# Kernel tuning notes

Hardware: AMD Instinct MI355X
Metric: run time of the kernel (lower is better)

## Reference

```python
import jax, jax.numpy as jnp
import numpy as np

B, S, D, H = 4, 4096, 128, 128

def setup_inputs() -> dict:
    key = jax.random.key(0)
    ks = jax.random.split(key, 7)
    sd = 1.0 / np.sqrt(D)
    return {
        "x": jax.random.normal(ks[0], (B, S, D), dtype=jnp.float32),
        "Wq": jax.random.normal(ks[1], (D, H), dtype=jnp.float32) * sd,
        "bq": jax.random.normal(ks[2], (H,), dtype=jnp.float32) * sd,
        "Wk": jax.random.normal(ks[3], (D, H), dtype=jnp.float32) * sd,
        "bk": jax.random.normal(ks[4], (H,), dtype=jnp.float32) * sd,
        "Wv": jax.random.normal(ks[5], (D, D), dtype=jnp.float32) * sd,
        "bv": jax.random.normal(ks[6], (D,), dtype=jnp.float32) * sd,
    }

def reference(x, Wq, bq, Wk, bk, Wv, bv):
    # Q,K: [B,S,H]; V: [B,S,D]
    Q = jnp.einsum('bsd,dh->bsh', x, Wq) + bq
    K = jnp.einsum('bsd,dh->bsh', x, Wk) + bk
    V = jnp.einsum('bsd,de->bse', x, Wv) + bv
    scale = jnp.sqrt(jnp.asarray(H, dtype=x.dtype))
    scores = jnp.einsum('bqh,bkh->bqk', Q, K) / scale  # [B,S,S]
    attn = jax.nn.softmax(scores, axis=-1)             # dropout = identity (eval mode)
    context = jnp.einsum('bqk,bkd->bqd', attn, V)      # [B,S,D]
    return context.mean(axis=1)                        # [B,D]
```

## Files before the change

kernel.cpp:

```cpp
#include <hip/hip_runtime.h>

#define SLEN 4096
#define DDIM 128
#define BATCH 4
#define KROWS 256
#define NKB (SLEN / KROWS)
#define QROWS 256
#define NQR (SLEN / QROWS)
#define NW 8
#define SCLOG2E 0.12751743f

typedef __bf16 v8bf __attribute__((ext_vector_type(8)));
typedef float f32x4 __attribute__((ext_vector_type(4)));

__device__ __forceinline__ f32x4 mfma16(v8bf a, v8bf b, f32x4 c) {
  return __builtin_amdgcn_mfma_f32_16x16x32_bf16(a, b, c, 0, 0, 0);
}

__device__ __forceinline__ void gload_lds16(const void* g, void* l) {
  __builtin_amdgcn_global_load_lds(
      (const __attribute__((address_space(1))) unsigned int*)g,
      (__attribute__((address_space(3))) unsigned int*)l, 16, 0, 0);
}

__device__ __forceinline__ void decode_bid(int bid, int& b, int& qr, int& kblk) {
  int x = bid & 7;
  int i = bid >> 3;
  int pr = x * 8 + (i >> 4);
  kblk = i & 15;
  b = pr >> 4;
  qr = pr & 15;
}

__device__ __forceinline__ void stage_kslab(const __bf16* __restrict__ Krow0,
                                            char* buf, int wave, int lane) {
#pragma unroll
  for (int it = 0; it < 8; ++it) {
    int s = it * 512 + wave * 64 + lane;
    int r = s >> 4;
    int pp = s & 15;
    int lsl = pp ^ (r & 7);
    const __bf16* src = Krow0 + (size_t)r * DDIM + lsl * 8;
    char* dst = buf + (size_t)(it * 512 + wave * 64) * 16;
    gload_lds16(src, dst);
  }
}

__device__ __forceinline__ void compute_tile(const char* kbuf, const v8bf qf[2][4],
                                             int lr, int lg, int kt, f32x4 A[2]) {
  int rowbase = (kt * 16 + lr) * 256;
#pragma unroll
  for (int qs = 0; qs < 2; ++qs) A[qs] = (f32x4){0.f, 0.f, 0.f, 0.f};
  __builtin_amdgcn_s_setprio(1);
#pragma unroll
  for (int hs = 0; hs < 4; ++hs) {
    int slot = (hs * 4 + lg) ^ (lr & 7);
    v8bf kc = *reinterpret_cast<const v8bf*>(kbuf + rowbase + slot * 16);
#pragma unroll
    for (int qs = 0; qs < 2; ++qs) A[qs] = mfma16(qf[qs][hs], kc, A[qs]);
  }
  __builtin_amdgcn_s_setprio(0);
}

__device__ __forceinline__ void consume_z(const f32x4 A[2], float zacc[2][4]) {
#pragma unroll
  for (int qs = 0; qs < 2; ++qs)
#pragma unroll
    for (int j = 0; j < 4; ++j)
      zacc[qs][j] += exp2f(A[qs][j]);
}

__global__ __launch_bounds__(256) void k0_wt(const float* __restrict__ Wq,
                                             const float* __restrict__ Wk,
                                             __bf16* __restrict__ Wt) {
  int idx = blockIdx.x * 256 + threadIdx.x;
  int ct = idx >> 8;
  int hs = (idx >> 6) & 3;
  int l  = idx & 63;
  int col = ((ct & 7) << 4) + (l & 15);
  const float* W = (ct < 8) ? Wq : Wk;
  int hbase = hs * 32 + (l >> 4) * 8;
  __bf16* dst = Wt + (size_t)idx * 8;
  for (int i = 0; i < 8; ++i)
    dst[i] = (__bf16)W[(hbase + i) * DDIM + col];
}

__global__ __launch_bounds__(256) void k1_proj(const float* __restrict__ x,
                                               const __bf16* __restrict__ Wt,
                                               const float* __restrict__ bq,
                                               const float* __restrict__ bk,
                                               __bf16* __restrict__ Qb,
                                               __bf16* __restrict__ Kb) {
  int wave = threadIdx.x >> 6, lane = threadIdx.x & 63;
  int lr = lane & 15, lg = lane >> 4;
  int r0 = blockIdx.x * 64 + wave * 16;
  const float* xrow = x + (size_t)(r0 + lr) * DDIM;

  v8bf xf[4];
#pragma unroll
  for (int hs = 0; hs < 4; ++hs) {
    float4 a = *reinterpret_cast<const float4*>(xrow + hs * 32 + lg * 8);
    float4 c = *reinterpret_cast<const float4*>(xrow + hs * 32 + lg * 8 + 4);
    v8bf t;
    t[0] = (__bf16)a.x; t[1] = (__bf16)a.y; t[2] = (__bf16)a.z; t[3] = (__bf16)a.w;
    t[4] = (__bf16)c.x; t[5] = (__bf16)c.y; t[6] = (__bf16)c.z; t[7] = (__bf16)c.w;
    xf[hs] = t;
  }

  for (int ct = 0; ct < 16; ++ct) {
    f32x4 acc = {0.f, 0.f, 0.f, 0.f};
#pragma unroll
    for (int hs = 0; hs < 4; ++hs) {
      v8bf wf = *reinterpret_cast<const v8bf*>(Wt + ((size_t)(ct * 4 + hs) * 64 + lane) * 8);
      acc = mfma16(xf[hs], wf, acc);
    }
    int col = ((ct & 7) << 4) + lr;
    float bias = (ct < 8) ? bq[col] : bk[col];
    float sc   = (ct < 8) ? SCLOG2E : 1.0f;
    __bf16* dst = (ct < 8) ? Qb : Kb;
#pragma unroll
    for (int j = 0; j < 4; ++j) {
      int row = r0 + lg * 4 + j;
      dst[(size_t)row * DDIM + col] = (__bf16)((acc[j] + bias) * sc);
    }
  }
}

__global__ __launch_bounds__(512, 4) void k2a_z(const __bf16* __restrict__ Qb,
                                                const __bf16* __restrict__ Kb,
                                                float* __restrict__ zpart) {
  int b, qr, kblk;
  decode_bid(blockIdx.x, b, qr, kblk);
  int p = b * NQR + qr;
  int wave = threadIdx.x >> 6, lane = threadIdx.x & 63;
  int lr = lane & 15, lg = lane >> 4;

  __shared__ __align__(16) char kbuf[KROWS * 256];

  stage_kslab(Kb + ((size_t)b * SLEN + kblk * KROWS) * DDIM, kbuf, wave, lane);

  int qloc0 = wave * 32;
  const __bf16* Qp = Qb + ((size_t)b * SLEN + qr * QROWS + qloc0) * DDIM;

  v8bf qf[2][4];
#pragma unroll
  for (int qs = 0; qs < 2; ++qs)
#pragma unroll
    for (int hs = 0; hs < 4; ++hs)
      qf[qs][hs] = *reinterpret_cast<const v8bf*>(Qp + (size_t)(qs * 16 + lr) * DDIM + hs * 32 + lg * 8);

  float zacc[2][4];
#pragma unroll
  for (int qs = 0; qs < 2; ++qs)
#pragma unroll
    for (int j = 0; j < 4; ++j) zacc[qs][j] = 0.f;

  __syncthreads();

  f32x4 a0[2], a1[2];
  compute_tile(kbuf, qf, lr, lg, 0, a0);
#pragma unroll 1
  for (int i = 0; i < 7; ++i) {
    compute_tile(kbuf, qf, lr, lg, 2 * i + 1, a1);
    consume_z(a0, zacc);
    compute_tile(kbuf, qf, lr, lg, 2 * i + 2, a0);
    consume_z(a1, zacc);
  }
  compute_tile(kbuf, qf, lr, lg, 15, a1);
  consume_z(a0, zacc);
  consume_z(a1, zacc);

#pragma unroll
  for (int qs = 0; qs < 2; ++qs)
#pragma unroll
    for (int j = 0; j < 4; ++j) {
      float z = zacc[qs][j];
      z += __shfl_xor(z, 1);
      z += __shfl_xor(z, 2);
      z += __shfl_xor(z, 4);
      z += __shfl_xor(z, 8);
      if (lr == 0)
        zpart[((size_t)p * NKB + kblk) * QROWS + qloc0 + qs * 16 + lg * 4 + j] = z;
    }
}

__global__ __launch_bounds__(512, 4) void k2c_w(const __bf16* __restrict__ Qb,
                                                const __bf16* __restrict__ Kb,
                                                const float* __restrict__ zpart,
                                                float* __restrict__ wpart) {
  int b, qr, kblk;
  decode_bid(blockIdx.x, b, qr, kblk);
  int p = b * NQR + qr;
  int wave = threadIdx.x >> 6, lane = threadIdx.x & 63;
  int lr = lane & 15, lg = lane >> 4;

  __shared__ __align__(16) char kbuf[KROWS * 256];
  __shared__ float invZ[QROWS];
  __shared__ float warr[NW][KROWS];

  stage_kslab(Kb + ((size_t)b * SLEN + kblk * KROWS) * DDIM, kbuf, wave, lane);

  if (threadIdx.x < QROWS) {
    const float* zp = zpart + (size_t)p * NKB * QROWS + threadIdx.x;
    float z = 0.f;
#pragma unroll
    for (int kb = 0; kb < NKB; ++kb) z += zp[(size_t)kb * QROWS];
    invZ[threadIdx.x] = 1.0f / z;
  }
  __syncthreads();

  int qloc0 = wave * 32;
  const __bf16* Qp = Qb + ((size_t)b * SLEN + qr * QROWS + qloc0) * DDIM;

  v8bf qf[2][4];
#pragma unroll
  for (int qs = 0; qs < 2; ++qs)
#pragma unroll
    for (int hs = 0; hs < 4; ++hs)
      qf[qs][hs] = *reinterpret_cast<const v8bf*>(Qp + (size_t)(qs * 16 + lr) * DDIM + hs * 32 + lg * 8);

  float iz[2][4];
#pragma unroll
  for (int qs = 0; qs < 2; ++qs)
#pragma unroll
    for (int j = 0; j < 4; ++j)
      iz[qs][j] = invZ[qloc0 + qs * 16 + lg * 4 + j];

  auto consume_w = [&](const f32x4 A[2], int kt) {
    float wk = 0.f;
#pragma unroll
    for (int qs = 0; qs < 2; ++qs)
#pragma unroll
      for (int j = 0; j < 4; ++j)
        wk += exp2f(A[qs][j]) * iz[qs][j];
    wk += __shfl_xor(wk, 16);
    wk += __shfl_xor(wk, 32);
    if (lg == 0) warr[wave][kt * 16 + lr] = wk;
  };

  f32x4 a0[2], a1[2];
  compute_tile(kbuf, qf, lr, lg, 0, a0);
#pragma unroll 1
  for (int i = 0; i < 7; ++i) {
    compute_tile(kbuf, qf, lr, lg, 2 * i + 1, a1);
    consume_w(a0, 2 * i);
    compute_tile(kbuf, qf, lr, lg, 2 * i + 2, a0);
    consume_w(a1, 2 * i + 1);
  }
  compute_tile(kbuf, qf, lr, lg, 15, a1);
  consume_w(a0, 14);
  consume_w(a1, 15);

  __syncthreads();
  if (threadIdx.x < KROWS) {
    int k = threadIdx.x;
    float s = 0.f;
#pragma unroll
    for (int w = 0; w < NW; ++w) s += warr[w][k];
    wpart[(size_t)p * SLEN + kblk * KROWS + k] = s;
  }
}

__global__ __launch_bounds__(256) void k4_u(const float* __restrict__ x,
                                            const float* __restrict__ wpart,
                                            float* __restrict__ upart) {
  int b = blockIdx.y, kc = blockIdx.x;
  int t = threadIdx.x;
  __shared__ float ws[256];
  {
    const float* pw = wpart + (size_t)b * NQR * SLEN + kc * 256 + t;
    float s = 0.f;
#pragma unroll
    for (int j = 0; j < NQR; ++j) s += pw[(size_t)j * SLEN];
    ws[t] = s;
  }
  __syncthreads();
  int d = t & 127, kh = t >> 7;
  const float* xb = x + ((size_t)b * SLEN + kc * 256 + kh * 128) * DDIM;
  float acc = 0.f;
  for (int kk = 0; kk < 128; ++kk)
    acc += ws[kh * 128 + kk] * xb[(size_t)kk * DDIM + d];
  upart[((size_t)b * 32 + kc * 2 + kh) * DDIM + d] = acc;
}

__global__ __launch_bounds__(128) void k5_out(const float* __restrict__ upart,
                                              const float* __restrict__ Wv,
                                              const float* __restrict__ bv,
                                              float* __restrict__ out) {
  int b = blockIdx.x, d = threadIdx.x;
  __shared__ float u[DDIM];
  float s = 0.f;
  for (int c = 0; c < 32; ++c) s += upart[((size_t)b * 32 + c) * DDIM + d];
  u[d] = s;
  __syncthreads();
  float acc = 0.f;
  for (int dp = 0; dp < DDIM; ++dp) acc += u[dp] * Wv[(size_t)dp * DDIM + d];
  out[b * DDIM + d] = acc * (1.0f / SLEN) + bv[d];
}

extern "C" void kernel_launch(void* const* d_in, const int* in_sizes, int n_in,
                              void* d_out, int out_size, void* d_ws, size_t ws_size,
                              hipStream_t stream) {
  const float* x  = (const float*)d_in[0];
  const float* Wq = (const float*)d_in[1];
  const float* bq = (const float*)d_in[2];
  const float* Wk = (const float*)d_in[3];
  const float* bk = (const float*)d_in[4];
  const float* Wv = (const float*)d_in[5];
  const float* bv = (const float*)d_in[6];
  float* out = (float*)d_out;

  char* ws = (char*)d_ws;
  __bf16* Qb    = (__bf16*)(ws);
  __bf16* Kb    = (__bf16*)(ws + (4u << 20));
  __bf16* Wt    = (__bf16*)(ws + (8u << 20));
  float*  zpart = (float*)(ws + (8u << 20) + (64u << 10));
  float*  wpart = (float*)(ws + (9u << 20) + (64u << 10));
  float*  upart = (float*)(ws + (10u << 20) + (64u << 10));

  k0_wt  <<<16, 256, 0, stream>>>(Wq, Wk, Wt);
  k1_proj<<<256, 256, 0, stream>>>(x, Wt, bq, bk, Qb, Kb);
  k2a_z  <<<NKB * NQR * BATCH, 512, 0, stream>>>(Qb, Kb, zpart);
  k2c_w  <<<NKB * NQR * BATCH, 512, 0, stream>>>(Qb, Kb, zpart, wpart);
  k4_u   <<<dim3(16, BATCH), 256, 0, stream>>>(x, wpart, upart);
  k5_out <<<BATCH, 128, 0, stream>>>(upart, Wv, bv, out);
}
```

Measured before the change: 79.92 us.

## Prefetch K fragments from LDS a tile ahead and stage Wt in LDS

In the z and w attention kernels, the K fragments for the next tile are now loaded from shared memory one tile ahead, into double-buffered registers, with LDS addresses precomputed per lane. This lets the LDS reads overlap the MFMA and exp work of the current tile, at the cost of extra VGPRs under launch_bounds(512,4). The setprio hints are dropped. Separately, the projection kernel copies the whole 64KB packed weight matrix into LDS with async global-to-LDS loads and reads it from there instead of from global memory, which uses a lot of LDS per block.

```diff
diff --git a/kernel.cpp b/kernel.cpp
--- a/kernel.cpp
+++ b/kernel.cpp
@@ -46,20 +46,22 @@
   }
 }
 
-__device__ __forceinline__ void compute_tile(const char* kbuf, const v8bf qf[2][4],
-                                             int lr, int lg, int kt, f32x4 A[2]) {
-  int rowbase = (kt * 16 + lr) * 256;
-#pragma unroll
-  for (int qs = 0; qs < 2; ++qs) A[qs] = (f32x4){0.f, 0.f, 0.f, 0.f};
-  __builtin_amdgcn_s_setprio(1);
-#pragma unroll
-  for (int hs = 0; hs < 4; ++hs) {
-    int slot = (hs * 4 + lg) ^ (lr & 7);
-    v8bf kc = *reinterpret_cast<const v8bf*>(kbuf + rowbase + slot * 16);
-#pragma unroll
-    for (int qs = 0; qs < 2; ++qs) A[qs] = mfma16(qf[qs][hs], kc, A[qs]);
-  }
-  __builtin_amdgcn_s_setprio(0);
+__device__ __forceinline__ void read4(v8bf k[4], const char* const pa[4], int t) {
+  int off = t << 12;
+#pragma unroll
+  for (int h = 0; h < 4; ++h)
+    k[h] = *reinterpret_cast<const v8bf*>(pa[h] + off);
+}
+
+__device__ __forceinline__ void mfma8(f32x4 A[2], const v8bf qf[2][4],
+                                      const v8bf k[4]) {
+  A[0] = (f32x4){0.f, 0.f, 0.f, 0.f};
+  A[1] = (f32x4){0.f, 0.f, 0.f, 0.f};
+#pragma unroll
+  for (int h = 0; h < 4; ++h) {
+    A[0] = mfma16(qf[0][h], k[h], A[0]);
+    A[1] = mfma16(qf[1][h], k[h], A[1]);
+  }
 }
 
 __device__ __forceinline__ void consume_z(const f32x4 A[2], float zacc[2][4]) {
@@ -93,6 +95,15 @@
                                                __bf16* __restrict__ Kb) {
   int wave = threadIdx.x >> 6, lane = threadIdx.x & 63;
   int lr = lane & 15, lg = lane >> 4;
+
+  __shared__ __align__(16) char wlds[64 * 1024];
+#pragma unroll
+  for (int it = 0; it < 16; ++it) {
+    int base = it * 256 + wave * 64;
+    gload_lds16((const char*)Wt + (size_t)(base + lane) * 16,
+                wlds + (size_t)base * 16);
+  }
+
   int r0 = blockIdx.x * 64 + wave * 16;
   const float* xrow = x + (size_t)(r0 + lr) * DDIM;
 
@@ -107,11 +118,14 @@
     xf[hs] = t;
   }
 
+  __syncthreads();
+
   for (int ct = 0; ct < 16; ++ct) {
     f32x4 acc = {0.f, 0.f, 0.f, 0.f};
 #pragma unroll
     for (int hs = 0; hs < 4; ++hs) {
-      v8bf wf = *reinterpret_cast<const v8bf*>(Wt + ((size_t)(ct * 4 + hs) * 64 + lane) * 8);
+      v8bf wf = *reinterpret_cast<const v8bf*>(
+          wlds + (size_t)((ct * 4 + hs) * 64 + lane) * 16);
       acc = mfma16(xf[hs], wf, acc);
     }
     int col = ((ct & 7) << 4) + lr;
@@ -149,6 +163,11 @@
     for (int hs = 0; hs < 4; ++hs)
       qf[qs][hs] = *reinterpret_cast<const v8bf*>(Qp + (size_t)(qs * 16 + lr) * DDIM + hs * 32 + lg * 8);
 
+  const char* pa[4];
+#pragma unroll
+  for (int hs = 0; hs < 4; ++hs)
+    pa[hs] = kbuf + lr * 256 + (((hs * 4 + lg) ^ (lr & 7)) << 4);
+
   float zacc[2][4];
 #pragma unroll
   for (int qs = 0; qs < 2; ++qs)
@@ -157,18 +176,23 @@
 
   __syncthreads();
 
-  f32x4 a0[2], a1[2];
-  compute_tile(kbuf, qf, lr, lg, 0, a0);
+  v8bf kA[4], kB[4];
+  f32x4 aA[2], aB[2];
+  read4(kA, pa, 0);
+  read4(kB, pa, 1);
+  mfma8(aA, qf, kA);
 #pragma unroll 1
   for (int i = 0; i < 7; ++i) {
-    compute_tile(kbuf, qf, lr, lg, 2 * i + 1, a1);
-    consume_z(a0, zacc);
-    compute_tile(kbuf, qf, lr, lg, 2 * i + 2, a0);
-    consume_z(a1, zacc);
-  }
-  compute_tile(kbuf, qf, lr, lg, 15, a1);
-  consume_z(a0, zacc);
-  consume_z(a1, zacc);
+    read4(kA, pa, 2 * i + 2);
+    mfma8(aB, qf, kB);
+    consume_z(aA, zacc);
+    read4(kB, pa, 2 * i + 3);
+    mfma8(aA, qf, kA);
+    consume_z(aB, zacc);
+  }
+  mfma8(aB, qf, kB);
+  consume_z(aA, zacc);
+  consume_z(aB, zacc);
 
 #pragma unroll
   for (int qs = 0; qs < 2; ++qs)
@@ -226,7 +250,14 @@
     for (int j = 0; j < 4; ++j)
       iz[qs][j] = invZ[qloc0 + qs * 16 + lg * 4 + j];
 
-  auto consume_w = [&](const f32x4 A[2], int kt) {
+  const char* pa[4];
+#pragma unroll
+  for (int hs = 0; hs < 4; ++hs)
+    pa[hs] = kbuf + lr * 256 + (((hs * 4 + lg) ^ (lr & 7)) << 4);
+
+  float* wbase = &warr[wave][lr];
+
+  auto cw = [&](const f32x4 A[2], int t) {
     float wk = 0.f;
 #pragma unroll
     for (int qs = 0; qs < 2; ++qs)
@@ -235,21 +266,26 @@
         wk += exp2f(A[qs][j]) * iz[qs][j];
     wk += __shfl_xor(wk, 16);
     wk += __shfl_xor(wk, 32);
-    if (lg == 0) warr[wave][kt * 16 + lr] = wk;
+    if (lg == 0) wbase[t * 16] = wk;
   };
 
-  f32x4 a0[2], a1[2];
-  compute_tile(kbuf, qf, lr, lg, 0, a0);
+  v8bf kA[4], kB[4];
+  f32x4 aA[2], aB[2];
+  read4(kA, pa, 0);
+  read4(kB, pa, 1);
+  mfma8(aA, qf, kA);
 #pragma unroll 1
   for (int i = 0; i < 7; ++i) {
-    compute_tile(kbuf, qf, lr, lg, 2 * i + 1, a1);
-    consume_w(a0, 2 * i);
-    compute_tile(kbuf, qf, lr, lg, 2 * i + 2, a0);
-    consume_w(a1, 2 * i + 1);
-  }
-  compute_tile(kbuf, qf, lr, lg, 15, a1);
-  consume_w(a0, 14);
-  consume_w(a1, 15);
+    read4(kA, pa, 2 * i + 2);
+    mfma8(aB, qf, kB);
+    cw(aA, 2 * i);
+    read4(kB, pa, 2 * i + 3);
+    mfma8(aA, qf, kA);
+    cw(aB, 2 * i + 1);
+  }
+  mfma8(aB, qf, kB);
+  cw(aA, 14);
+  cw(aB, 15);
 
   __syncthreads();
   if (threadIdx.x < KROWS) {
```

New measurement: 76.49 us. 4.3% less time.
